# Kernel optimization log

Measured on AMD Instinct MI355X. Metric: run time of the kernel, lower is better.

Reference implementation:

```python
import jax, jax.numpy as jnp
import numpy as np

LEAKY_SLOPE = 0.2  # tf.nn.leaky_relu default alpha


def setup_inputs() -> dict:
    key = jax.random.key(0)
    k1, k2, k3 = jax.random.split(key, 3)
    B, T, K, D = 64, 2048, 256, 256  # batch, timesteps, n_nodes, out_dim
    inputs = jax.random.normal(k1, (B, T, K), dtype=jnp.float32)
    W = jax.random.normal(k2, (K, D), dtype=jnp.float32) * (1.0 / np.sqrt(K))
    a = jax.random.normal(k3, (2 * D, 1), dtype=jnp.float32) * (1.0 / np.sqrt(2 * D))
    return {"inputs": inputs, "W": W, "a": a}


def reference(inputs, W, a):
    # inputs: (B, T, K); W: (K, D); a: (2D, 1)
    B, T, K = inputs.shape
    D = W.shape[1]
    H = jnp.matmul(inputs, W)  # (B, T, D)
    # Original: H_concat[b,t,k] = concat([H[b,t], H[b,t]]) for every k (both
    # repeats are of the same H), so H_concat @ a == H @ (a_i + a_j), constant in k.
    a_i = a[:D, 0]
    a_j = a[D:, 0]
    e = jax.nn.leaky_relu(H @ (a_i + a_j), negative_slope=LEAKY_SLOPE)  # (B, T)
    e = jnp.broadcast_to(e[:, :, None], (B, T, K))  # (B, T, K) -- constant along K
    alpha = jax.nn.softmax(e, axis=2)  # exactly uniform 1/K
    # sum_k alpha[b,t,k] * H[b,t,d]  (H_repeat_i[b,t,k,:] == H[b,t,:])
    H_gat = jnp.einsum('btk,btd->btd', alpha, H)  # (B, T, D)
    return H_gat
```

## Files before the change

### kernel.cpp

```cpp
#include <hip/hip_runtime.h>
#include <hip/hip_bf16.h>
#include <cstdint>


static constexpr int MTOT = 64 * 2048;
static constexpr int KDIM = 256;
static constexpr int NDIM = 256;

typedef __bf16 bf16x8 __attribute__((ext_vector_type(8)));
typedef float f32x4 __attribute__((ext_vector_type(4)));

__device__ __forceinline__ uint32_t f2bf_pk(float a, float b) {
    uint32_t ua = __float_as_uint(a);
    uint32_t ub = __float_as_uint(b);
    ua = ua + 0x7fffu + ((ua >> 16) & 1u);
    ub = ub + 0x7fffu + ((ub >> 16) & 1u);
    return (ua >> 16) | (ub & 0xffff0000u);
}

__global__ void wt_transpose(const float* __restrict__ W, unsigned short* __restrict__ Wt) {
    int n = blockIdx.x;
    int k = threadIdx.x;
    float v = W[k * NDIM + n];
    uint32_t u = __float_as_uint(v);
    u = u + 0x7fffu + ((u >> 16) & 1u);
    Wt[n * KDIM + k] = (unsigned short)(u >> 16);
}

__global__ __launch_bounds__(512, 4)
void gat_gemm(const float* __restrict__ A, const unsigned short* __restrict__ Wt,
              float* __restrict__ C) {
    __shared__ alignas(16) unsigned short As[128 * 72];
    __shared__ alignas(16) unsigned short Bs[256 * 72];

    const int tid  = threadIdx.x;
    const int lane = tid & 63;
    const int wave = tid >> 6;
    const int l15  = lane & 15;
    const int quad = lane >> 4;
    const int wm   = wave >> 2;
    const int wn   = wave & 3;

    const int bm = blockIdx.x * 128;

    const int arow = tid >> 2;
    const int aseg = tid & 3;
    const int brow = tid >> 3;
    const int bseg = tid & 7;

    f32x4 acc[4][4];
#pragma unroll
    for (int i = 0; i < 4; ++i)
#pragma unroll
        for (int j = 0; j < 4; ++j)
            acc[i][j] = (f32x4)0.0f;

    for (int kt = 0; kt < 4; ++kt) {
        const int k0 = kt * 64;

        const float4* ap = (const float4*)(A + (size_t)(bm + arow) * KDIM + k0 + aseg * 16);
        float4 a0 = ap[0], a1 = ap[1], a2 = ap[2], a3 = ap[3];

        const unsigned short* bp = Wt + (size_t)brow * KDIM + k0 + bseg * 8;
        uint4 b0 = *(const uint4*)(bp);
        uint4 b1 = *(const uint4*)(bp + 64 * KDIM);
        uint4 b2 = *(const uint4*)(bp + 128 * KDIM);
        uint4 b3 = *(const uint4*)(bp + 192 * KDIM);

        if (kt) __syncthreads();

        {
            uint4 w0, w1;
            w0.x = f2bf_pk(a0.x, a0.y); w0.y = f2bf_pk(a0.z, a0.w);
            w0.z = f2bf_pk(a1.x, a1.y); w0.w = f2bf_pk(a1.z, a1.w);
            w1.x = f2bf_pk(a2.x, a2.y); w1.y = f2bf_pk(a2.z, a2.w);
            w1.z = f2bf_pk(a3.x, a3.y); w1.w = f2bf_pk(a3.z, a3.w);
            uint4* dst = (uint4*)&As[arow * 72 + aseg * 16];
            dst[0] = w0;
            dst[1] = w1;
        }
        *(uint4*)&Bs[(brow +   0) * 72 + bseg * 8] = b0;
        *(uint4*)&Bs[(brow +  64) * 72 + bseg * 8] = b1;
        *(uint4*)&Bs[(brow + 128) * 72 + bseg * 8] = b2;
        *(uint4*)&Bs[(brow + 192) * 72 + bseg * 8] = b3;

        __syncthreads();

#pragma unroll
        for (int ks = 0; ks < 2; ++ks) {
            bf16x8 af[4];
#pragma unroll
            for (int i = 0; i < 4; ++i)
                af[i] = *(const bf16x8*)&As[(wm * 64 + i * 16 + l15) * 72 + ks * 32 + quad * 8];
#pragma unroll
            for (int j = 0; j < 4; ++j) {
                bf16x8 bfj = *(const bf16x8*)&Bs[(wn * 64 + j * 16 + l15) * 72 + ks * 32 + quad * 8];
#pragma unroll
                for (int i = 0; i < 4; ++i)
                    acc[i][j] = __builtin_amdgcn_mfma_f32_16x16x32_bf16(af[i], bfj, acc[i][j], 0, 0, 0);
            }
        }
    }

#pragma unroll
    for (int i = 0; i < 4; ++i) {
#pragma unroll
        for (int j = 0; j < 4; ++j) {
            const int n = wn * 64 + j * 16 + l15;
            const size_t mbase = (size_t)(bm + wm * 64 + i * 16 + quad * 4);
#pragma unroll
            for (int r = 0; r < 4; ++r)
                C[(mbase + r) * NDIM + n] = acc[i][j][r];
        }
    }
}

extern "C" void kernel_launch(void* const* d_in, const int* in_sizes, int n_in,
                              void* d_out, int out_size, void* d_ws, size_t ws_size,
                              hipStream_t stream) {
    (void)in_sizes; (void)n_in; (void)out_size; (void)ws_size;
    const float* inputs = (const float*)d_in[0];
    const float* W      = (const float*)d_in[1];
    unsigned short* Wt = (unsigned short*)d_ws;
    float* out = (float*)d_out;

    hipLaunchKernelGGL(wt_transpose, dim3(NDIM), dim3(KDIM), 0, stream, W, Wt);
    hipLaunchKernelGGL(gat_gemm, dim3(MTOT / 128), dim3(512), 0, stream, inputs, Wt, out);
}
```

Baseline: 243.1 us.

## Keep whole bf16 W in swizzled LDS and stream A rows per wave

The GEMM kernel now loads the entire transposed bf16 weight matrix (128 KB) into XOR-swizzled shared memory once per block. Each wave then processes 64 rows in four 16-row steps, loading A straight from global memory into registers and prefetching the next step while the current one computes. This removes the per-k-tile LDS staging of A and the repeated block barriers, and each block covers 512 rows, so W is reloaded less often. In exchange, the 128 KB of LDS limits occupancy to about one block per CU, A loads are strided rather than coalesced, and the per-row output stores are narrow.

```diff
diff --git a/kernel.cpp b/kernel.cpp
--- a/kernel.cpp
+++ b/kernel.cpp
@@ -1,5 +1,4 @@
 #include <hip/hip_runtime.h>
-#include <hip/hip_bf16.h>
 #include <cstdint>
 
 
@@ -27,90 +26,84 @@
     Wt[n * KDIM + k] = (unsigned short)(u >> 16);
 }
 
-__global__ __launch_bounds__(512, 4)
+__global__ __launch_bounds__(512, 2)
 void gat_gemm(const float* __restrict__ A, const unsigned short* __restrict__ Wt,
               float* __restrict__ C) {
-    __shared__ alignas(16) unsigned short As[128 * 72];
-    __shared__ alignas(16) unsigned short Bs[256 * 72];
+    __shared__ alignas(16) unsigned short Bs[256 * 256];
 
     const int tid  = threadIdx.x;
     const int lane = tid & 63;
     const int wave = tid >> 6;
     const int l15  = lane & 15;
     const int quad = lane >> 4;
-    const int wm   = wave >> 2;
-    const int wn   = wave & 3;
 
-    const int bm = blockIdx.x * 128;
+    const int mwave = blockIdx.x * 512 + wave * 64;
 
-    const int arow = tid >> 2;
-    const int aseg = tid & 3;
-    const int brow = tid >> 3;
-    const int bseg = tid & 7;
-
-    f32x4 acc[4][4];
+    float4 abuf[16];
+    {
+        const float* ap = A + (size_t)(mwave + l15) * KDIM + quad * 8;
 #pragma unroll
-    for (int i = 0; i < 4; ++i)
-#pragma unroll
-        for (int j = 0; j < 4; ++j)
-            acc[i][j] = (f32x4)0.0f;
-
-    for (int kt = 0; kt < 4; ++kt) {
-        const int k0 = kt * 64;
-
-        const float4* ap = (const float4*)(A + (size_t)(bm + arow) * KDIM + k0 + aseg * 16);
-        float4 a0 = ap[0], a1 = ap[1], a2 = ap[2], a3 = ap[3];
-
-        const unsigned short* bp = Wt + (size_t)brow * KDIM + k0 + bseg * 8;
-        uint4 b0 = *(const uint4*)(bp);
-        uint4 b1 = *(const uint4*)(bp + 64 * KDIM);
-        uint4 b2 = *(const uint4*)(bp + 128 * KDIM);
-        uint4 b3 = *(const uint4*)(bp + 192 * KDIM);
-
-        if (kt) __syncthreads();
-
-        {
-            uint4 w0, w1;
-            w0.x = f2bf_pk(a0.x, a0.y); w0.y = f2bf_pk(a0.z, a0.w);
-            w0.z = f2bf_pk(a1.x, a1.y); w0.w = f2bf_pk(a1.z, a1.w);
-            w1.x = f2bf_pk(a2.x, a2.y); w1.y = f2bf_pk(a2.z, a2.w);
-            w1.z = f2bf_pk(a3.x, a3.y); w1.w = f2bf_pk(a3.z, a3.w);
-            uint4* dst = (uint4*)&As[arow * 72 + aseg * 16];
-            dst[0] = w0;
-            dst[1] = w1;
-        }
-        *(uint4*)&Bs[(brow +   0) * 72 + bseg * 8] = b0;
-        *(uint4*)&Bs[(brow +  64) * 72 + bseg * 8] = b1;
-        *(uint4*)&Bs[(brow + 128) * 72 + bseg * 8] = b2;
-        *(uint4*)&Bs[(brow + 192) * 72 + bseg * 8] = b3;
-
-        __syncthreads();
-
-#pragma unroll
-        for (int ks = 0; ks < 2; ++ks) {
-            bf16x8 af[4];
-#pragma unroll
-            for (int i = 0; i < 4; ++i)
-                af[i] = *(const bf16x8*)&As[(wm * 64 + i * 16 + l15) * 72 + ks * 32 + quad * 8];
-#pragma unroll
-            for (int j = 0; j < 4; ++j) {
-                bf16x8 bfj = *(const bf16x8*)&Bs[(wn * 64 + j * 16 + l15) * 72 + ks * 32 + quad * 8];
-#pragma unroll
-                for (int i = 0; i < 4; ++i)
-                    acc[i][j] = __builtin_amdgcn_mfma_f32_16x16x32_bf16(af[i], bfj, acc[i][j], 0, 0, 0);
-            }
+        for (int ks = 0; ks < 8; ++ks) {
+            abuf[2 * ks]     = *(const float4*)(ap + ks * 32);
+            abuf[2 * ks + 1] = *(const float4*)(ap + ks * 32 + 4);
         }
     }
 
 #pragma unroll
-    for (int i = 0; i < 4; ++i) {
+    for (int c = 0; c < 16; ++c) {
+        int idx = c * 512 + tid;
+        int n   = idx >> 5;
+        int kc  = idx & 31;
+        uint4 v = *(const uint4*)(Wt + (size_t)idx * 8);
+        int dst = n * 512 + ((kc * 16) ^ ((n & 7) << 4));
+        *(uint4*)((char*)Bs + dst) = v;
+    }
+    __syncthreads();
+
+#pragma unroll 1
+    for (int s = 0; s < 4; ++s) {
+        bf16x8 af[8];
 #pragma unroll
-        for (int j = 0; j < 4; ++j) {
-            const int n = wn * 64 + j * 16 + l15;
-            const size_t mbase = (size_t)(bm + wm * 64 + i * 16 + quad * 4);
+        for (int ks = 0; ks < 8; ++ks) {
+            float4 lo = abuf[2 * ks], hi = abuf[2 * ks + 1];
+            uint4 w;
+            w.x = f2bf_pk(lo.x, lo.y); w.y = f2bf_pk(lo.z, lo.w);
+            w.z = f2bf_pk(hi.x, hi.y); w.w = f2bf_pk(hi.z, hi.w);
+            af[ks] = *(bf16x8*)&w;
+        }
+
+        if (s < 3) {
+            const float* ap = A + (size_t)(mwave + (s + 1) * 16 + l15) * KDIM + quad * 8;
 #pragma unroll
-            for (int r = 0; r < 4; ++r)
-                C[(mbase + r) * NDIM + n] = acc[i][j][r];
+            for (int ks = 0; ks < 8; ++ks) {
+                abuf[2 * ks]     = *(const float4*)(ap + ks * 32);
+                abuf[2 * ks + 1] = *(const float4*)(ap + ks * 32 + 4);
+            }
+        }
+
+        f32x4 acc[16];
+#pragma unroll
+        for (int j = 0; j < 16; ++j) acc[j] = (f32x4)0.0f;
+
+#pragma unroll
+        for (int ks = 0; ks < 8; ++ks) {
+            const int kbyte = ks * 64 + quad * 16;
+#pragma unroll
+            for (int j = 0; j < 16; ++j) {
+                const int n = j * 16 + l15;
+                bf16x8 bf = *(const bf16x8*)((const char*)Bs +
+                              n * 512 + (kbyte ^ ((n & 7) << 4)));
+                acc[j] = __builtin_amdgcn_mfma_f32_16x16x32_bf16(af[ks], bf, acc[j], 0, 0, 0);
+            }
+        }
+
+        const size_t mbase = (size_t)(mwave + s * 16 + quad * 4);
+#pragma unroll
+        for (int r = 0; r < 4; ++r) {
+            float* cp = C + (mbase + r) * NDIM + l15;
+#pragma unroll
+            for (int j = 0; j < 16; ++j)
+                cp[j * 16] = acc[j][r];
         }
     }
 }
@@ -125,5 +118,5 @@
     float* out = (float*)d_out;
 
     hipLaunchKernelGGL(wt_transpose, dim3(NDIM), dim3(KDIM), 0, stream, W, Wt);
-    hipLaunchKernelGGL(gat_gemm, dim3(MTOT / 128), dim3(512), 0, stream, inputs, Wt, out);
+    hipLaunchKernelGGL(gat_gemm, dim3(MTOT / 512), dim3(512), 0, stream, inputs, Wt, out);
 }
```

Result: slower. 505.9 us (+108.1%).
